# Kernel tuning notes

Measured on AMD Instinct MI355X. Metric: run time of the kernel, lower is better.

## Reference

```python
import jax, jax.numpy as jnp
import numpy as np

D_MODEL = 1024
NUM_HEADS = 16
D_K = D_MODEL // NUM_HEADS
NEG_INF = -1e9


def setup_inputs() -> dict:
    key = jax.random.key(0)
    ks = jax.random.split(key, 12)
    B, S = 2, 2048
    Q = jax.random.normal(ks[0], (B, S, D_MODEL), jnp.float32)
    K = jax.random.normal(ks[1], (B, S, D_MODEL), jnp.float32)
    V = jax.random.normal(ks[2], (B, S, D_MODEL), jnp.float32)
    mask = jax.random.randint(ks[3], (B, 1, 1, S), 0, 2, jnp.int32)
    scale = 1.0 / np.sqrt(D_MODEL)
    WQ = jax.random.normal(ks[4], (D_MODEL, D_MODEL), jnp.float32) * scale
    bQ = jnp.zeros((D_MODEL,), jnp.float32)
    WK = jax.random.normal(ks[5], (D_MODEL, D_MODEL), jnp.float32) * scale
    bK = jnp.zeros((D_MODEL,), jnp.float32)
    WV = jax.random.normal(ks[6], (D_MODEL, D_MODEL), jnp.float32) * scale
    bV = jnp.zeros((D_MODEL,), jnp.float32)
    WO = jax.random.normal(ks[7], (D_MODEL, D_MODEL), jnp.float32) * scale
    bO = jnp.zeros((D_MODEL,), jnp.float32)
    return {"Q": Q, "K": K, "V": V, "mask": mask,
            "WQ": WQ, "bQ": bQ, "WK": WK, "bK": bK,
            "WV": WV, "bV": bV, "WO": WO, "bO": bO}


def _split_heads(x):
    # (B, S, d_model) -> (B, H, S, d_k)
    B, S, _ = x.shape
    return x.reshape(B, S, NUM_HEADS, D_K).transpose(0, 2, 1, 3)


def reference(Q, K, V, mask, WQ, bQ, WK, bK, WV, bV, WO, bO):
    B, Sq, _ = Q.shape
    q = _split_heads(Q @ WQ + bQ)   # (B, H, Sq, d_k)
    k = _split_heads(K @ WK + bK)   # (B, H, Sk, d_k)
    v = _split_heads(V @ WV + bV)   # (B, H, Sk, d_v)
    scores = jnp.einsum('bhqd,bhkd->bhqk', q, k) / jnp.sqrt(jnp.float32(D_K))
    scores = jnp.where(mask == 0, jnp.float32(NEG_INF), scores)
    attention = jax.nn.softmax(scores, axis=-1)         # (B, H, Sq, Sk)
    context = jnp.einsum('bhqk,bhkd->bhqd', attention, v)
    context = context.transpose(0, 2, 1, 3).reshape(B, Sq, D_MODEL)
    output = context @ WO + bO
    return (output, attention)
```

## Files before the change

### kernel.cpp

```cpp
#include <hip/hip_runtime.h>

typedef __attribute__((ext_vector_type(8))) __bf16 bf16x8;
typedef __attribute__((ext_vector_type(4))) float f32x4;
typedef __attribute__((ext_vector_type(8))) unsigned short u16x8;

#define DEVFN static __device__ __forceinline__

#if __has_builtin(__builtin_amdgcn_exp2f)
#define EXP2(x) __builtin_amdgcn_exp2f(x)
#else
#define EXP2(x) exp2f(x)
#endif

DEVFN f32x4 mfma16(bf16x8 a, bf16x8 b, f32x4 c) {
  return __builtin_amdgcn_mfma_f32_16x16x32_bf16(a, b, c, 0, 0, 0);
}

DEVFN void gload16(const void* g, void* l) {
  __builtin_amdgcn_global_load_lds((const __attribute__((address_space(1))) void*)g,
                                   (__attribute__((address_space(3))) void*)l, 16, 0, 0);
}

__global__ __launch_bounds__(256) void cvt2_k(const float* __restrict__ s0,
                                              unsigned short* __restrict__ d0,
                                              const float* __restrict__ s1,
                                              unsigned short* __restrict__ d1) {
  const float* in = blockIdx.z ? s1 : s0;
  unsigned short* out = blockIdx.z ? d1 : d0;
  int i = blockIdx.x * 256 + threadIdx.x;
  int e0 = i << 3;
  int row = e0 >> 10, col0 = e0 & 1023;
  const float4* s = (const float4*)(in + ((size_t)row << 10) + col0);
  float4 a = s[0], b = s[1];
  bf16x8 o;
  o[0] = (__bf16)a.x; o[1] = (__bf16)a.y; o[2] = (__bf16)a.z; o[3] = (__bf16)a.w;
  o[4] = (__bf16)b.x; o[5] = (__bf16)b.y; o[6] = (__bf16)b.z; o[7] = (__bf16)b.w;
  size_t ob = ((size_t)row << 11) + (size_t)((col0 << 1) ^ ((row & 7) << 4));
  *(bf16x8*)((char*)out + ob) = o;
}

__global__ __launch_bounds__(256) void transW4(const float* __restrict__ w0,
                                               const float* __restrict__ w1,
                                               const float* __restrict__ w2,
                                               const float* __restrict__ w3,
                                               unsigned short* __restrict__ obase) {
  __shared__ float t[64][65];
  const float* W = blockIdx.z == 0 ? w0 : blockIdx.z == 1 ? w1 : blockIdx.z == 2 ? w2 : w3;
  unsigned short* Wt = obase + ((size_t)blockIdx.z << 20);
  int k0 = blockIdx.x * 64, n0 = blockIdx.y * 64;
  int tid = threadIdx.x;
#pragma unroll
  for (int it = 0; it < 4; ++it) {
    int r = it * 16 + (tid >> 4);
    int c = (tid & 15) * 4;
    float4 v = *(const float4*)(W + (size_t)(k0 + r) * 1024 + n0 + c);
    t[r][c] = v.x; t[r][c + 1] = v.y; t[r][c + 2] = v.z; t[r][c + 3] = v.w;
  }
  __syncthreads();
#pragma unroll
  for (int it = 0; it < 2; ++it) {
    int nl = it * 32 + (tid >> 3);
    int kc = tid & 7;
    bf16x8 o;
#pragma unroll
    for (int j = 0; j < 8; ++j) o[j] = (__bf16)t[kc * 8 + j][nl];
    int n = n0 + nl;
    char* dst = (char*)Wt + (size_t)n * 2048 + (k0 << 1) + ((kc ^ (n & 7)) << 4);
    *(bf16x8*)dst = o;
  }
}

struct GArg {
  const unsigned short* A;
  const unsigned short* Bt;
  const float* bias;
  unsigned short* outH;
  float* outF;
  float scale;
};

template <int BM, int BN, int WR, int WC, int MODE>
__global__ __launch_bounds__(256, 2) void gemm_t(GArg g0, GArg g1) {
  GArg g = (blockIdx.z == 0) ? g0 : g1;
  constexpr int MT = BM / WR / 16, NT = BN / WC / 16;
  __shared__ unsigned short lA[BM * 64];
  __shared__ unsigned short lB[BN * 64];
  int tid = threadIdx.x, wave = tid >> 6, lane = tid & 63;
  int hi = lane >> 4, lo = lane & 15;
  int m0 = blockIdx.x * BM, n0 = blockIdx.y * BN;
  int wr = wave / WC, wc = wave % WC;
  f32x4 acc[MT][NT];
#pragma unroll
  for (int mt = 0; mt < MT; ++mt)
#pragma unroll
    for (int nt = 0; nt < NT; ++nt) acc[mt][nt] = (f32x4){0.f, 0.f, 0.f, 0.f};

  for (int k0 = 0; k0 < 1024; k0 += 64) {
#pragma unroll
    for (int i = 0; i < BM / 32; ++i) {
      int off = i * 4096 + tid * 16;
      int row = off >> 7, colb = off & 127;
      gload16((const char*)g.A + (size_t)(m0 + row) * 2048 + (k0 << 1) + colb,
              (char*)lA + i * 4096 + wave * 1024);
    }
#pragma unroll
    for (int i = 0; i < BN / 32; ++i) {
      int off = i * 4096 + tid * 16;
      int row = off >> 7, colb = off & 127;
      gload16((const char*)g.Bt + (size_t)(n0 + row) * 2048 + (k0 << 1) + colb,
              (char*)lB + i * 4096 + wave * 1024);
    }
    __syncthreads();
#pragma unroll
    for (int kk = 0; kk < 2; ++kk) {
      bf16x8 af[MT], bfr[NT];
#pragma unroll
      for (int mt = 0; mt < MT; ++mt) {
        int row = wr * (BM / WR) + mt * 16 + lo;
        int ob = (row << 7) + ((((kk << 2) + hi) << 4) ^ ((row & 7) << 4));
        af[mt] = *(const bf16x8*)((const char*)lA + ob);
      }
#pragma unroll
      for (int nt = 0; nt < NT; ++nt) {
        int row = wc * (BN / WC) + nt * 16 + lo;
        int ob = (row << 7) + ((((kk << 2) + hi) << 4) ^ ((row & 7) << 4));
        bfr[nt] = *(const bf16x8*)((const char*)lB + ob);
      }
#pragma unroll
      for (int mt = 0; mt < MT; ++mt)
#pragma unroll
        for (int nt = 0; nt < NT; ++nt)
          acc[mt][nt] = mfma16(af[mt], bfr[nt], acc[mt][nt]);
    }
    __syncthreads();
  }
#pragma unroll
  for (int mt = 0; mt < MT; ++mt) {
#pragma unroll
    for (int nt = 0; nt < NT; ++nt) {
      int col = n0 + wc * (BN / WC) + nt * 16 + lo;
      float bs = g.bias[col];
#pragma unroll
      for (int j = 0; j < 4; ++j) {
        int row = m0 + wr * (BM / WR) + mt * 16 + (hi << 2) + j;
        float v = (acc[mt][nt][j] + bs) * g.scale;
        if (MODE == 1) {
          g.outF[(size_t)row * 1024 + col] = v;
        } else {
          size_t hb = ((size_t)((row >> 11) * 16 + (col >> 6))) << 18;
          int ib = ((row & 2047) << 7) + ((col & 63) << 1);
          ib ^= (row & 7) << 4;
          *(__bf16*)((char*)g.outH + hb + ib) = (__bf16)v;
        }
      }
    }
  }
}

__global__ __launch_bounds__(256) void transV(const unsigned short* __restrict__ vh,
                                              unsigned short* __restrict__ vt) {
  __shared__ unsigned short t[64][72];
  int k0 = blockIdx.x * 64;
  int bh = blockIdx.y;
  int tid = threadIdx.x;
  const char* head = (const char*)vh + ((size_t)bh << 18);
#pragma unroll
  for (int it = 0; it < 2; ++it) {
    int off = it * 4096 + tid * 16;
    int r = off >> 7, cb = off & 127;
    u16x8 v = *(const u16x8*)(head + (size_t)(k0 + r) * 128 + (cb ^ ((r & 7) << 4)));
    *(u16x8*)&t[r][cb >> 1] = v;
  }
  __syncthreads();
  char* ohead = (char*)vt + ((size_t)bh << 18);
#pragma unroll
  for (int it = 0; it < 2; ++it) {
    int d = it * 32 + (tid >> 3);
    int kc = tid & 7;
    u16x8 o;
#pragma unroll
    for (int j = 0; j < 8; ++j) o[j] = t[kc * 8 + j][d];
    *(u16x8*)(ohead + (size_t)d * 4096 + (k0 << 1) + ((kc ^ (d & 7)) << 4)) = o;
  }
}

__global__ __launch_bounds__(256, 4) void attn_k(
    const unsigned short* __restrict__ qh, const unsigned short* __restrict__ kh,
    const unsigned short* __restrict__ vt, const int* __restrict__ mask,
    float* __restrict__ attn, unsigned short* __restrict__ ctx) {
  constexpr int S = 2048;
  __shared__ unsigned short ktl[64 * 64];
  __shared__ unsigned short vtl[64 * 64];
  __shared__ unsigned long long mkb[32];
  __shared__ float pf[4][16 * 68];

  int tid = threadIdx.x, wave = tid >> 6, lane = tid & 63;
  int hi = lane >> 4, lo = lane & 15;
  int f = blockIdx.y * 32 + blockIdx.x;
  int xcd = f & 7, slot = f >> 3;
  int bh = xcd * 4 + (slot & 3);
  int qb = slot >> 2;
  int b = bh >> 4, h = bh & 15;
  const char* khead = (const char*)kh + ((size_t)bh << 18);
  const char* qhead = (const char*)qh + ((size_t)bh << 18);
  const char* vhead = (const char*)vt + ((size_t)bh << 18);

  for (int it = 0; it < 8; ++it) {
    unsigned long long bal = __ballot(mask[b * S + it * 256 + tid] != 0);
    if (lane == 0) mkb[it * 4 + wave] = bal;
  }
  __syncthreads();

  int q0 = qb * 64 + wave * 16;
  bf16x8 qf[2];
  {
    int row = q0 + lo;
#pragma unroll
    for (int kk = 0; kk < 2; ++kk) {
      int ib = (row << 7) + ((((kk << 2) + hi) << 4) ^ ((row & 7) << 4));
      qf[kk] = *(const bf16x8*)(qhead + ib);
    }
  }

  float lsum[4] = {0.f, 0.f, 0.f, 0.f};

  for (int kt = 0; kt < 32; ++kt) {
#pragma unroll
    for (int i = 0; i < 2; ++i)
      gload16(khead + (size_t)kt * 8192 + i * 4096 + tid * 16,
              (char*)ktl + i * 4096 + wave * 1024);
    __syncthreads();
    unsigned long long mw = mkb[kt];
    __builtin_amdgcn_s_setprio(1);
#pragma unroll
    for (int nt = 0; nt < 4; ++nt) {
      int r = nt * 16 + lo;
      f32x4 a = {0.f, 0.f, 0.f, 0.f};
#pragma unroll
      for (int kk = 0; kk < 2; ++kk) {
        int ob = (r << 7) + ((((kk << 2) + hi) << 4) ^ ((r & 7) << 4));
        a = mfma16(qf[kk], *(const bf16x8*)((const char*)ktl + ob), a);
      }
      bool ok = (mw >> r) & 1ull;
#pragma unroll
      for (int j = 0; j < 4; ++j) lsum[j] += ok ? EXP2(a[j]) : 0.f;
    }
    __builtin_amdgcn_s_setprio(0);
    __syncthreads();
  }

  float rcp[4];
#pragma unroll
  for (int j = 0; j < 4; ++j) {
    float s = lsum[j];
    s += __shfl_xor(s, 1); s += __shfl_xor(s, 2);
    s += __shfl_xor(s, 4); s += __shfl_xor(s, 8);
    rcp[j] = s > 0.f ? 1.0f / s : 0.f;
  }

  f32x4 cacc[4];
#pragma unroll
  for (int nt = 0; nt < 4; ++nt) cacc[nt] = (f32x4){0.f, 0.f, 0.f, 0.f};

  float* arow = attn + (size_t)bh * S * S;
  float* pfw = pf[wave];

  for (int kt = 0; kt < 32; ++kt) {
#pragma unroll
    for (int i = 0; i < 2; ++i)
      gload16(khead + (size_t)kt * 8192 + i * 4096 + tid * 16,
              (char*)ktl + i * 4096 + wave * 1024);
#pragma unroll
    for (int i = 0; i < 2; ++i) {
      int off = i * 4096 + tid * 16;
      int d = off >> 7, x = off & 127;
      gload16(vhead + (size_t)d * 4096 + kt * 128 + x,
              (char*)vtl + i * 4096 + wave * 1024);
    }
    __syncthreads();
    unsigned long long mw = mkb[kt];
    __builtin_amdgcn_s_setprio(1);
#pragma unroll
    for (int nt = 0; nt < 4; ++nt) {
      int r = nt * 16 + lo;
      f32x4 a = {0.f, 0.f, 0.f, 0.f};
#pragma unroll
      for (int kk = 0; kk < 2; ++kk) {
        int ob = (r << 7) + ((((kk << 2) + hi) << 4) ^ ((r & 7) << 4));
        a = mfma16(qf[kk], *(const bf16x8*)((const char*)ktl + ob), a);
      }
      bool ok = (mw >> r) & 1ull;
#pragma unroll
      for (int j = 0; j < 4; ++j) {
        float pn = ok ? EXP2(a[j]) * rcp[j] : 0.f;
        pfw[((hi << 2) + j) * 68 + r] = pn;
      }
    }
#pragma unroll
    for (int c = 0; c < 2; ++c) {
      f32x4 p0 = *(const f32x4*)&pfw[lo * 68 + c * 32 + hi * 8];
      f32x4 p1 = *(const f32x4*)&pfw[lo * 68 + c * 32 + hi * 8 + 4];
      bf16x8 pa;
#pragma unroll
      for (int i = 0; i < 4; ++i) { pa[i] = (__bf16)p0[i]; pa[4 + i] = (__bf16)p1[i]; }
#pragma unroll
      for (int nt = 0; nt < 4; ++nt) {
        int d = nt * 16 + lo;
        int ob = (d << 7) + ((((c << 2) + hi) << 4) ^ ((d & 7) << 4));
        cacc[nt] = mfma16(pa, *(const bf16x8*)((const char*)vtl + ob), cacc[nt]);
      }
    }
    __builtin_amdgcn_s_setprio(0);
    {
      int rsub = lane >> 4;
      int cb = (lane & 15) << 2;
      float* dst0 = arow + (size_t)q0 * S + kt * 64 + cb;
      const float* src0 = pfw + rsub * 68 + cb;
#pragma unroll
      for (int s = 0; s < 4; ++s) {
        int row = s * 4 + rsub;
        f32x4 v = *(const f32x4*)(src0 + s * 4 * 68);
        __builtin_nontemporal_store(v, (f32x4*)(dst0 + (size_t)row * S - (size_t)rsub * S + (size_t)rsub * S));
      }
    }
    __syncthreads();
  }

#pragma unroll
  for (int nt = 0; nt < 4; ++nt) {
#pragma unroll
    for (int j = 0; j < 4; ++j) {
      int s = q0 + (hi << 2) + j;
      int mrow = b * S + s;
      int n = h * 64 + nt * 16 + lo;
      int ib = (n << 1) ^ ((mrow & 7) << 4);
      *(__bf16*)((char*)ctx + (size_t)mrow * 2048 + ib) = (__bf16)cacc[nt][j];
    }
  }
}

extern "C" void kernel_launch(void* const* d_in, const int* in_sizes, int n_in,
                              void* d_out, int out_size, void* d_ws, size_t ws_size,
                              hipStream_t stream) {
  const float* Q  = (const float*)d_in[0];
  const float* K  = (const float*)d_in[1];
  const float* V  = (const float*)d_in[2];
  const int* mask = (const int*)d_in[3];
  const float* WQ = (const float*)d_in[4];
  const float* bQ = (const float*)d_in[5];
  const float* WK = (const float*)d_in[6];
  const float* bK = (const float*)d_in[7];
  const float* WV = (const float*)d_in[8];
  const float* bV = (const float*)d_in[9];
  const float* WO = (const float*)d_in[10];
  const float* bO = (const float*)d_in[11];

  char* ws = (char*)d_ws;
  const size_t M1 = 1ull << 20;
  unsigned short* WQt = (unsigned short*)(ws + 0 * M1);
  unsigned short* WKt = (unsigned short*)(ws + 2 * M1);
  unsigned short* WVt = (unsigned short*)(ws + 4 * M1);
  unsigned short* WOt = (unsigned short*)(ws + 6 * M1);
  unsigned short* qh  = (unsigned short*)(ws + 8 * M1);
  unsigned short* kh  = (unsigned short*)(ws + 16 * M1);
  unsigned short* vh  = (unsigned short*)(ws + 24 * M1);
  unsigned short* Qb  = (unsigned short*)(ws + 32 * M1);
  unsigned short* Kb  = (unsigned short*)(ws + 40 * M1);
  unsigned short* Vb  = (unsigned short*)(ws + 32 * M1);
  unsigned short* vt  = (unsigned short*)(ws + 40 * M1);
  unsigned short* ctx = (unsigned short*)(ws + 32 * M1);

  float* outF = (float*)d_out;
  float* attn = (float*)d_out + 4194304;

  dim3 blk(256);
  const float qscale = 0.125f * 1.44269504088896340736f;

  cvt2_k<<<dim3(2048, 1, 2), blk, 0, stream>>>(Q, Qb, K, Kb);
  transW4<<<dim3(16, 16, 4), blk, 0, stream>>>(WQ, WK, WV, WO, WQt);

  GArg aq{Qb, WQt, bQ, qh, nullptr, qscale};
  GArg ak{Kb, WKt, bK, kh, nullptr, 1.f};
  gemm_t<128, 128, 2, 2, 0><<<dim3(32, 8, 2), blk, 0, stream>>>(aq, ak);

  cvt2_k<<<dim3(2048, 1, 1), blk, 0, stream>>>(V, Vb, V, Vb);

  GArg av{Vb, WVt, bV, vh, nullptr, 1.f};
  gemm_t<64, 128, 1, 4, 0><<<dim3(64, 8, 1), blk, 0, stream>>>(av, av);

  transV<<<dim3(32, 32), blk, 0, stream>>>(vh, vt);

  attn_k<<<dim3(32, 32), blk, 0, stream>>>(qh, kh, vt, mask, attn, ctx);

  GArg ao{ctx, WOt, bO, nullptr, outF, 1.f};
  gemm_t<64, 128, 1, 4, 1><<<dim3(64, 8, 1), blk, 0, stream>>>(ao, ao);
}
```

Before: 257.1 us.

## Fuse fp32-to-bf16 conversion and V transpose into a single QKV projection GEMM

```diff
diff --git a/kernel.cpp b/kernel.cpp
--- a/kernel.cpp
+++ b/kernel.cpp
@@ -1,8 +1,8 @@
 #include <hip/hip_runtime.h>
 
 typedef __attribute__((ext_vector_type(8))) __bf16 bf16x8;
+typedef __attribute__((ext_vector_type(4))) __bf16 bf16x4;
 typedef __attribute__((ext_vector_type(4))) float f32x4;
-typedef __attribute__((ext_vector_type(8))) unsigned short u16x8;
 
 #define DEVFN static __device__ __forceinline__
 
@@ -19,24 +19,6 @@
 DEVFN void gload16(const void* g, void* l) {
   __builtin_amdgcn_global_load_lds((const __attribute__((address_space(1))) void*)g,
                                    (__attribute__((address_space(3))) void*)l, 16, 0, 0);
-}
-
-__global__ __launch_bounds__(256) void cvt2_k(const float* __restrict__ s0,
-                                              unsigned short* __restrict__ d0,
-                                              const float* __restrict__ s1,
-                                              unsigned short* __restrict__ d1) {
-  const float* in = blockIdx.z ? s1 : s0;
-  unsigned short* out = blockIdx.z ? d1 : d0;
-  int i = blockIdx.x * 256 + threadIdx.x;
-  int e0 = i << 3;
-  int row = e0 >> 10, col0 = e0 & 1023;
-  const float4* s = (const float4*)(in + ((size_t)row << 10) + col0);
-  float4 a = s[0], b = s[1];
-  bf16x8 o;
-  o[0] = (__bf16)a.x; o[1] = (__bf16)a.y; o[2] = (__bf16)a.z; o[3] = (__bf16)a.w;
-  o[4] = (__bf16)b.x; o[5] = (__bf16)b.y; o[6] = (__bf16)b.z; o[7] = (__bf16)b.w;
-  size_t ob = ((size_t)row << 11) + (size_t)((col0 << 1) ^ ((row & 7) << 4));
-  *(bf16x8*)((char*)out + ob) = o;
 }
 
 __global__ __launch_bounds__(256) void transW4(const float* __restrict__ w0,
@@ -71,20 +53,20 @@
 }
 
 struct GArg {
-  const unsigned short* A;
+  const void* A;
   const unsigned short* Bt;
   const float* bias;
-  unsigned short* outH;
-  float* outF;
+  void* out;
   float scale;
 };
 
-template <int BM, int BN, int WR, int WC, int MODE>
-__global__ __launch_bounds__(256, 2) void gemm_t(GArg g0, GArg g1) {
-  GArg g = (blockIdx.z == 0) ? g0 : g1;
+template <int BM, int BN, int WR, int WC, int AF32, int EPI>
+__global__ __launch_bounds__(256, 2) void gemm_t(GArg g0, GArg g1, GArg g2) {
+  GArg g = blockIdx.z == 0 ? g0 : blockIdx.z == 1 ? g1 : g2;
   constexpr int MT = BM / WR / 16, NT = BN / WC / 16;
-  __shared__ unsigned short lA[BM * 64];
-  __shared__ unsigned short lB[BN * 64];
+  constexpr int AB = AF32 ? 4 : 2;
+  __shared__ char lA[BM * 64 * AB];
+  __shared__ char lB[BN * 64 * 2];
   int tid = threadIdx.x, wave = tid >> 6, lane = tid & 63;
   int hi = lane >> 4, lo = lane & 15;
   int m0 = blockIdx.x * BM, n0 = blockIdx.y * BN;
@@ -96,19 +78,30 @@
     for (int nt = 0; nt < NT; ++nt) acc[mt][nt] = (f32x4){0.f, 0.f, 0.f, 0.f};
 
   for (int k0 = 0; k0 < 1024; k0 += 64) {
-#pragma unroll
-    for (int i = 0; i < BM / 32; ++i) {
-      int off = i * 4096 + tid * 16;
-      int row = off >> 7, colb = off & 127;
-      gload16((const char*)g.A + (size_t)(m0 + row) * 2048 + (k0 << 1) + colb,
-              (char*)lA + i * 4096 + wave * 1024);
+    if (AF32) {
+#pragma unroll
+      for (int i = 0; i < BM / 16; ++i) {
+        int off = i * 4096 + tid * 16;
+        int row = off >> 8, b = off & 255;
+        gload16((const char*)g.A + (size_t)(m0 + row) * 4096 + (k0 << 2)
+                    + (b ^ ((row & 7) << 4)),
+                lA + i * 4096 + wave * 1024);
+      }
+    } else {
+#pragma unroll
+      for (int i = 0; i < BM / 32; ++i) {
+        int off = i * 4096 + tid * 16;
+        int row = off >> 7, b = off & 127;
+        gload16((const char*)g.A + (size_t)(m0 + row) * 2048 + (k0 << 1) + b,
+                lA + i * 4096 + wave * 1024);
+      }
     }
 #pragma unroll
     for (int i = 0; i < BN / 32; ++i) {
       int off = i * 4096 + tid * 16;
-      int row = off >> 7, colb = off & 127;
-      gload16((const char*)g.Bt + (size_t)(n0 + row) * 2048 + (k0 << 1) + colb,
-              (char*)lB + i * 4096 + wave * 1024);
+      int row = off >> 7, b = off & 127;
+      gload16((const char*)g.Bt + (size_t)(n0 + row) * 2048 + (k0 << 1) + b,
+              lB + i * 4096 + wave * 1024);
     }
     __syncthreads();
 #pragma unroll
@@ -117,14 +110,25 @@
 #pragma unroll
       for (int mt = 0; mt < MT; ++mt) {
         int row = wr * (BM / WR) + mt * 16 + lo;
-        int ob = (row << 7) + ((((kk << 2) + hi) << 4) ^ ((row & 7) << 4));
-        af[mt] = *(const bf16x8*)((const char*)lA + ob);
+        if (AF32) {
+          int base = (row << 8) + ((kk << 7) + (hi << 5));
+          int sw = (row & 7) << 4;
+          f32x4 a0 = *(const f32x4*)(lA + ((base) ^ sw));
+          f32x4 a1 = *(const f32x4*)(lA + ((base + 16) ^ sw));
+          bf16x8 v;
+#pragma unroll
+          for (int j = 0; j < 4; ++j) { v[j] = (__bf16)a0[j]; v[4 + j] = (__bf16)a1[j]; }
+          af[mt] = v;
+        } else {
+          int ob = (row << 7) + ((((kk << 2) + hi) << 4) ^ ((row & 7) << 4));
+          af[mt] = *(const bf16x8*)(lA + ob);
+        }
       }
 #pragma unroll
       for (int nt = 0; nt < NT; ++nt) {
         int row = wc * (BN / WC) + nt * 16 + lo;
         int ob = (row << 7) + ((((kk << 2) + hi) << 4) ^ ((row & 7) << 4));
-        bfr[nt] = *(const bf16x8*)((const char*)lB + ob);
+        bfr[nt] = *(const bf16x8*)(lB + ob);
       }
 #pragma unroll
       for (int mt = 0; mt < MT; ++mt)
@@ -134,53 +138,42 @@
     }
     __syncthreads();
   }
+
 #pragma unroll
   for (int mt = 0; mt < MT; ++mt) {
 #pragma unroll
     for (int nt = 0; nt < NT; ++nt) {
       int col = n0 + wc * (BN / WC) + nt * 16 + lo;
       float bs = g.bias[col];
-#pragma unroll
-      for (int j = 0; j < 4; ++j) {
-        int row = m0 + wr * (BM / WR) + mt * 16 + (hi << 2) + j;
-        float v = (acc[mt][nt][j] + bs) * g.scale;
-        if (MODE == 1) {
-          g.outF[(size_t)row * 1024 + col] = v;
-        } else {
-          size_t hb = ((size_t)((row >> 11) * 16 + (col >> 6))) << 18;
-          int ib = ((row & 2047) << 7) + ((col & 63) << 1);
-          ib ^= (row & 7) << 4;
-          *(__bf16*)((char*)g.outH + hb + ib) = (__bf16)v;
+      int row0 = m0 + wr * (BM / WR) + mt * 16 + (hi << 2);
+      float vj[4];
+#pragma unroll
+      for (int j = 0; j < 4; ++j) vj[j] = (acc[mt][nt][j] + bs) * g.scale;
+      if (EPI == 1) {
+#pragma unroll
+        for (int j = 0; j < 4; ++j)
+          ((float*)g.out)[(size_t)(row0 + j) * 1024 + col] = vj[j];
+      } else if (blockIdx.z == 2) {
+        int d = col & 63;
+        int bh = (row0 >> 11) * 16 + (col >> 6);
+        int s = row0 & 2047;
+        bf16x4 o;
+#pragma unroll
+        for (int j = 0; j < 4; ++j) o[j] = (__bf16)vj[j];
+        char* p = (char*)g.out + ((size_t)bh << 18) + (size_t)d * 4096
+                  + (s >> 6) * 128 + (((((s & 63) >> 3) ^ (d & 7)) << 4))
+                  + ((s & 7) << 1);
+        *(bf16x4*)p = o;
+      } else {
+#pragma unroll
+        for (int j = 0; j < 4; ++j) {
+          int srow = row0 + j;
+          size_t hb = ((size_t)((srow >> 11) * 16 + (col >> 6))) << 18;
+          int ib = ((srow & 2047) << 7) + (((col & 63) << 1) ^ ((srow & 7) << 4));
+          *(__bf16*)((char*)g.out + hb + ib) = (__bf16)vj[j];
         }
       }
     }
-  }
-}
-
-__global__ __launch_bounds__(256) void transV(const unsigned short* __restrict__ vh,
-                                              unsigned short* __restrict__ vt) {
-  __shared__ unsigned short t[64][72];
-  int k0 = blockIdx.x * 64;
-  int bh = blockIdx.y;
-  int tid = threadIdx.x;
-  const char* head = (const char*)vh + ((size_t)bh << 18);
-#pragma unroll
-  for (int it = 0; it < 2; ++it) {
-    int off = it * 4096 + tid * 16;
-    int r = off >> 7, cb = off & 127;
-    u16x8 v = *(const u16x8*)(head + (size_t)(k0 + r) * 128 + (cb ^ ((r & 7) << 4)));
-    *(u16x8*)&t[r][cb >> 1] = v;
-  }
-  __syncthreads();
-  char* ohead = (char*)vt + ((size_t)bh << 18);
-#pragma unroll
-  for (int it = 0; it < 2; ++it) {
-    int d = it * 32 + (tid >> 3);
-    int kc = tid & 7;
-    u16x8 o;
-#pragma unroll
-    for (int j = 0; j < 8; ++j) o[j] = t[kc * 8 + j][d];
-    *(u16x8*)(ohead + (size_t)d * 4096 + (k0 << 1) + ((kc ^ (d & 7)) << 4)) = o;
   }
 }
 
@@ -224,12 +217,23 @@
 
   float lsum[4] = {0.f, 0.f, 0.f, 0.f};
 
+#pragma unroll
+  for (int i = 0; i < 2; ++i)
+    gload16(khead + i * 4096 + tid * 16, (char*)ktl + i * 4096 + wave * 1024);
   for (int kt = 0; kt < 32; ++kt) {
-#pragma unroll
-    for (int i = 0; i < 2; ++i)
-      gload16(khead + (size_t)kt * 8192 + i * 4096 + tid * 16,
-              (char*)ktl + i * 4096 + wave * 1024);
-    __syncthreads();
+    const char* cb = (kt & 1) ? (const char*)vtl : (const char*)ktl;
+    char* nb = (kt & 1) ? (char*)ktl : (char*)vtl;
+    if (kt < 31) {
+#pragma unroll
+      for (int i = 0; i < 2; ++i)
+        gload16(khead + (size_t)(kt + 1) * 8192 + i * 4096 + tid * 16,
+                nb + i * 4096 + wave * 1024);
+      asm volatile("s_waitcnt vmcnt(2)" ::: "memory");
+    } else {
+      asm volatile("s_waitcnt vmcnt(0)" ::: "memory");
+    }
+    __builtin_amdgcn_sched_barrier(0);
+    __builtin_amdgcn_s_barrier();
     unsigned long long mw = mkb[kt];
     __builtin_amdgcn_s_setprio(1);
 #pragma unroll
@@ -239,14 +243,14 @@
 #pragma unroll
       for (int kk = 0; kk < 2; ++kk) {
         int ob = (r << 7) + ((((kk << 2) + hi) << 4) ^ ((r & 7) << 4));
-        a = mfma16(qf[kk], *(const bf16x8*)((const char*)ktl + ob), a);
+        a = mfma16(qf[kk], *(const bf16x8*)(cb + ob), a);
       }
       bool ok = (mw >> r) & 1ull;
 #pragma unroll
       for (int j = 0; j < 4; ++j) lsum[j] += ok ? EXP2(a[j]) : 0.f;
     }
     __builtin_amdgcn_s_setprio(0);
-    __syncthreads();
+    __builtin_amdgcn_s_barrier();
   }
 
   float rcp[4];
@@ -314,13 +318,12 @@
     {
       int rsub = lane >> 4;
       int cb = (lane & 15) << 2;
-      float* dst0 = arow + (size_t)q0 * S + kt * 64 + cb;
-      const float* src0 = pfw + rsub * 68 + cb;
 #pragma unroll
       for (int s = 0; s < 4; ++s) {
         int row = s * 4 + rsub;
-        f32x4 v = *(const f32x4*)(src0 + s * 4 * 68);
-        __builtin_nontemporal_store(v, (f32x4*)(dst0 + (size_t)row * S - (size_t)rsub * S + (size_t)rsub * S));
+        f32x4 v = *(const f32x4*)&pfw[row * 68 + cb];
+        __builtin_nontemporal_store(
+            v, (f32x4*)(arow + (size_t)(q0 + row) * S + kt * 64 + cb));
       }
     }
     __syncthreads();
@@ -363,11 +366,7 @@
   unsigned short* WOt = (unsigned short*)(ws + 6 * M1);
   unsigned short* qh  = (unsigned short*)(ws + 8 * M1);
   unsigned short* kh  = (unsigned short*)(ws + 16 * M1);
-  unsigned short* vh  = (unsigned short*)(ws + 24 * M1);
-  unsigned short* Qb  = (unsigned short*)(ws + 32 * M1);
-  unsigned short* Kb  = (unsigned short*)(ws + 40 * M1);
-  unsigned short* Vb  = (unsigned short*)(ws + 32 * M1);
-  unsigned short* vt  = (unsigned short*)(ws + 40 * M1);
+  unsigned short* vt  = (unsigned short*)(ws + 24 * M1);
   unsigned short* ctx = (unsigned short*)(ws + 32 * M1);
 
   float* outF = (float*)d_out;
@@ -376,22 +375,15 @@
   dim3 blk(256);
   const float qscale = 0.125f * 1.44269504088896340736f;
 
-  cvt2_k<<<dim3(2048, 1, 2), blk, 0, stream>>>(Q, Qb, K, Kb);
   transW4<<<dim3(16, 16, 4), blk, 0, stream>>>(WQ, WK, WV, WO, WQt);
 
-  GArg aq{Qb, WQt, bQ, qh, nullptr, qscale};
-  GArg ak{Kb, WKt, bK, kh, nullptr, 1.f};
-  gemm_t<128, 128, 2, 2, 0><<<dim3(32, 8, 2), blk, 0, stream>>>(aq, ak);
-
-  cvt2_k<<<dim3(2048, 1, 1), blk, 0, stream>>>(V, Vb, V, Vb);
-
-  GArg av{Vb, WVt, bV, vh, nullptr, 1.f};
-  gemm_t<64, 128, 1, 4, 0><<<dim3(64, 8, 1), blk, 0, stream>>>(av, av);
-
-  transV<<<dim3(32, 32), blk, 0, stream>>>(vh, vt);
+  GArg aq{Q, WQt, bQ, qh, qscale};
+  GArg ak{K, WKt, bK, kh, 1.f};
+  GArg av{V, WVt, bV, vt, 1.f};
+  gemm_t<128, 128, 2, 2, 1, 0><<<dim3(32, 8, 3), blk, 0, stream>>>(aq, ak, av);
 
   attn_k<<<dim3(32, 32), blk, 0, stream>>>(qh, kh, vt, mask, attn, ctx);
 
-  GArg ao{ctx, WOt, bO, nullptr, outF, 1.f};
-  gemm_t<64, 128, 1, 4, 1><<<dim3(64, 8, 1), blk, 0, stream>>>(ao, ao);
-}
+  GArg ao{ctx, WOt, bO, outF, 1.f};
+  gemm_t<64, 128, 1, 4, 0, 1><<<dim3(64, 8, 1), blk, 0, stream>>>(ao, ao, ao);
+}
```

Measured after the change: 246.4 us. -4.2%, faster.
